# Kernel tuning notes

Measured on AMD Instinct MI355X. Metric: run time of the kernel, lower is better.

Reference implementation:

```python
import jax, jax.numpy as jnp
import numpy as np
import math

B, T, C, H = 4, 1024, 1024, 16
D = C // H
EPS = 1e-5

def layer_norm(x, gamma, beta):
    mu = jnp.mean(x, axis=-1, keepdims=True)
    var = jnp.var(x, axis=-1, keepdims=True)
    return (x - mu) * jax.lax.rsqrt(var + EPS) * gamma + beta

def setup_inputs() -> dict:
    key = jax.random.key(0)
    ks = jax.random.split(key, 12)
    s = 0.02
    return {
        "x": jax.random.normal(ks[0], (B, T, C), dtype=jnp.float32),
        "attn_mask": jax.random.randint(ks[1], (B, 1, 1, T), 0, 2, dtype=jnp.int32),
        "Wq": jax.random.normal(ks[2], (C, C), dtype=jnp.float32) * s,
        "bq": jnp.zeros((C,), dtype=jnp.float32),
        "Wk": jax.random.normal(ks[3], (C, C), dtype=jnp.float32) * s,
        "bk": jnp.zeros((C,), dtype=jnp.float32),
        "Wv": jax.random.normal(ks[4], (C, C), dtype=jnp.float32) * s,
        "bv": jnp.zeros((C,), dtype=jnp.float32),
        "Wo": jax.random.normal(ks[5], (C, C), dtype=jnp.float32) * s,
        "bo": jnp.zeros((C,), dtype=jnp.float32),
        "ln_g": jnp.ones((C,), dtype=jnp.float32),
        "ln_b": jnp.zeros((C,), dtype=jnp.float32),
    }

def reference(x, attn_mask, Wq, bq, Wk, bk, Wv, bv, Wo, bo, ln_g, ln_b):
    # projections -> [B, H, T, D]
    def split_heads(y):
        return y.reshape(B, T, H, D).transpose(0, 2, 1, 3)
    q = split_heads(x @ Wq + bq)
    k = split_heads(x @ Wk + bk)
    v = split_heads(x @ Wv + bv)
    scale = 1.0 / math.sqrt(D)
    wei = jnp.einsum('bhqd,bhkd->bhqk', q, k) * scale  # [B,H,T,T]
    wei = jnp.where(attn_mask == 0, jnp.float32(-jnp.inf), wei)
    wei = jax.nn.softmax(wei, axis=-1)
    out = jnp.einsum('bhqk,bhkd->bhqd', wei, v)
    out = out.transpose(0, 2, 1, 3).reshape(B, T, C)
    out = out @ Wo + bo
    return layer_norm(out, ln_g, ln_b)
```

## Files before the change

kernel.cpp:

```cpp
#include <hip/hip_runtime.h>
#include <stdint.h>

#define B_ 4
#define T_ 1024
#define C_ 1024
#define H_ 16
#define D_ 64
#define M_ 4096

typedef __attribute__((ext_vector_type(8))) short bf16x8;
typedef __attribute__((ext_vector_type(4))) float f32x4;
typedef __attribute__((ext_vector_type(4))) short short4v;

static __device__ __forceinline__ short f2bf(float f) {
  union { float f; unsigned u; } c; c.f = f;
  unsigned r = (c.u + 0x7fffu + ((c.u >> 16) & 1u)) >> 16;
  return (short)(unsigned short)r;
}

static __device__ __forceinline__ void gl2lds16(const void* g, void* l) {
  __builtin_amdgcn_global_load_lds(
      (const __attribute__((address_space(1))) void*)(uintptr_t)g,
      (__attribute__((address_space(3))) void*)(uint32_t)(uintptr_t)l,
      16, 0, 0);
}

__global__ __launch_bounds__(256) void k_prep(
    const float* __restrict__ x, short* __restrict__ xb,
    const float* __restrict__ Wq, const float* __restrict__ Wk,
    const float* __restrict__ Wv, const float* __restrict__ Wo,
    short* __restrict__ Wt) {
  __shared__ float t[32][33];
  const int id = blockIdx.x, tid = threadIdx.x;
  if (id < 4096) {
    int i = id * 256 + tid;
    float4 v = ((const float4*)x)[i];
    short4v o;
    o.x = f2bf(v.x); o.y = f2bf(v.y); o.z = f2bf(v.z); o.w = f2bf(v.w);
    ((short4v*)xb)[i] = o;
    return;
  }
  int j = id - 4096;
  int bz = j >> 10, r = j & 1023;
  int by = r >> 5, bx = r & 31;
  const float* W = (bz == 0) ? Wq : (bz == 1) ? Wk : (bz == 2) ? Wv : Wo;
  short* out = Wt + (size_t)bz * C_ * C_;
  int n0 = bx * 32, k0 = by * 32;
  int tx = tid & 31, ty = tid >> 5;
#pragma unroll
  for (int i = 0; i < 4; i++)
    t[ty + 8*i][tx] = W[(size_t)(k0 + ty + 8*i) * C_ + n0 + tx];
  __syncthreads();
#pragma unroll
  for (int i = 0; i < 4; i++)
    out[(size_t)(n0 + ty + 8*i) * C_ + k0 + tx] = f2bf(t[tx][ty + 8*i]);
}

static __device__ __forceinline__ void gemm_body(const short* __restrict__ A,
                                                 const short* __restrict__ Bt,
                                                 short* sA, short* sB,
                                                 f32x4 acc[4][4], int m0, int n0) {
  const int tid = threadIdx.x;
  const int w = tid >> 6, lane = tid & 63;
  const int quad = lane >> 4, l16 = lane & 15;
  const int wm = (w >> 1) * 64, wn = (w & 1) * 64;
  const int srow = lane >> 3;
  const int sch = lane & 7;

#pragma unroll
  for (int mt = 0; mt < 4; mt++)
#pragma unroll
    for (int nt = 0; nt < 4; nt++)
#pragma unroll
      for (int e = 0; e < 4; e++) acc[mt][nt][e] = 0.f;

  for (int k0 = 0; k0 < C_; k0 += 64) {
    __syncthreads();
#pragma unroll
    for (int i = 0; i < 4; i++) {
      int c = w * 4 + i;
      int row = c * 8 + srow;
      int ch = sch ^ (row & 7);
      gl2lds16(&A[(size_t)(m0 + row) * C_ + k0 + ch * 8], &sA[c * 512]);
      gl2lds16(&Bt[(size_t)(n0 + row) * C_ + k0 + ch * 8], &sB[c * 512]);
    }
    __syncthreads();
#pragma unroll
    for (int ks = 0; ks < 2; ks++) {
      bf16x8 af[4], bfv[4];
      int chq = ks * 4 + quad;
#pragma unroll
      for (int t4 = 0; t4 < 4; t4++) {
        int rowa = wm + t4 * 16 + l16;
        af[t4] = *(const bf16x8*)&sA[rowa * 64 + (chq ^ (rowa & 7)) * 8];
        int rowb = wn + t4 * 16 + l16;
        bfv[t4] = *(const bf16x8*)&sB[rowb * 64 + (chq ^ (rowb & 7)) * 8];
      }
#pragma unroll
      for (int mt = 0; mt < 4; mt++)
#pragma unroll
        for (int nt = 0; nt < 4; nt++)
          acc[mt][nt] = __builtin_amdgcn_mfma_f32_16x16x32_bf16(
              af[mt], bfv[nt], acc[mt][nt], 0, 0, 0);
    }
  }
}

__global__ __launch_bounds__(256, 3) void k_qkv(
    const short* __restrict__ A, const short* __restrict__ WtAll,
    const float* __restrict__ bq, const float* __restrict__ bk,
    const float* __restrict__ bv,
    short* __restrict__ Qb, short* __restrict__ Kb, short* __restrict__ Vtb) {
  __shared__ short sU[17408];
  const int id = blockIdx.x;
  const int mode = id % 3;
  const int j = id / 3;
  const int bx = j & 7, by = j >> 3;
  const int m0 = by * 128, n0 = bx * 128;
  const short* Bt = WtAll + (size_t)mode * C_ * C_;
  const float* bias = (mode == 0) ? bq : (mode == 1) ? bk : bv;
  f32x4 acc[4][4];
  gemm_body(A, Bt, sU, sU + 8192, acc, m0, n0);

  const int tid = threadIdx.x;
  const int w = tid >> 6, lane = tid & 63;
  const int quad = lane >> 4, l16 = lane & 15;
  const int wm = (w >> 1) * 64, wn = (w & 1) * 64;

  __syncthreads();
  if (mode < 2) {
#pragma unroll
    for (int nt = 0; nt < 4; nt++) {
      int nl = wn + nt * 16 + l16;
      float bval = bias[n0 + nl];
#pragma unroll
      for (int mt = 0; mt < 4; mt++)
#pragma unroll
        for (int r = 0; r < 4; r++)
          sU[(wm + mt * 16 + quad * 4 + r) * 136 + nl] = f2bf(acc[mt][nt][r] + bval);
    }
    __syncthreads();
    int dr = tid >> 1, hf = tid & 1;
    int mg = m0 + dr;
    int bb = mg >> 10, t = mg & 1023;
    int h = (n0 >> 6) + hf;
    short* dst = (mode == 0) ? Qb : Kb;
    size_t base = ((((size_t)(bb * H_ + h)) << 10) + t) * D_;
#pragma unroll
    for (int i = 0; i < 8; i++)
      *(int4*)&dst[base + i * 8] = *(const int4*)&sU[dr * 136 + hf * 64 + i * 8];
  } else {
#pragma unroll
    for (int nt = 0; nt < 4; nt++) {
      int nl = wn + nt * 16 + l16;
      float bval = bias[n0 + nl];
#pragma unroll
      for (int mt = 0; mt < 4; mt++)
#pragma unroll
        for (int r = 0; r < 4; r++)
          sU[nl * 136 + wm + mt * 16 + quad * 4 + r] = f2bf(acc[mt][nt][r] + bval);
    }
    __syncthreads();
    int dr = tid >> 1;
    int dg = n0 + dr, hd = dg >> 6, dl = dg & 63;
    int bb2 = m0 >> 10, t0 = m0 & 1023;
    size_t base = (((size_t)(bb2 * H_ + hd) * D_ + dl) << 10) + t0;
#pragma unroll
    for (int i = 0; i < 8; i++) {
      int jj = (tid & 1) * 8 + i;
      *(int4*)&Vtb[base + jj * 8] = *(const int4*)&sU[dr * 136 + jj * 8];
    }
  }
}

__global__ __launch_bounds__(256) void k_proj(
    const short* __restrict__ A, const short* __restrict__ Bt,
    const float* __restrict__ bias, float* __restrict__ Y) {
  __shared__ short sA[4096];
  __shared__ short sB[8192];
  const int tid = threadIdx.x;
  const int w = tid >> 6, lane = tid & 63;
  const int quad = lane >> 4, l16 = lane & 15;
  const int m0 = blockIdx.y * 64, n0 = blockIdx.x * 128;
  const int wm = (w >> 1) * 32, wn = (w & 1) * 64;
  const int srow = lane >> 3, sch = lane & 7;

  f32x4 acc[2][4];
#pragma unroll
  for (int mt = 0; mt < 2; mt++)
#pragma unroll
    for (int nt = 0; nt < 4; nt++)
#pragma unroll
      for (int e = 0; e < 4; e++) acc[mt][nt][e] = 0.f;

  for (int k0 = 0; k0 < C_; k0 += 64) {
    __syncthreads();
#pragma unroll
    for (int i = 0; i < 6; i++) {
      int c = w * 6 + i;
      if (c < 8) {
        int row = c * 8 + srow;
        int ch = sch ^ (row & 7);
        gl2lds16(&A[(size_t)(m0 + row) * C_ + k0 + ch * 8], &sA[c * 512]);
      } else {
        int c2 = c - 8;
        int row = c2 * 8 + srow;
        int ch = sch ^ (row & 7);
        gl2lds16(&Bt[(size_t)(n0 + row) * C_ + k0 + ch * 8], &sB[c2 * 512]);
      }
    }
    __syncthreads();
#pragma unroll
    for (int ks = 0; ks < 2; ks++) {
      bf16x8 af[2], bfv[4];
      int chq = ks * 4 + quad;
#pragma unroll
      for (int t2 = 0; t2 < 2; t2++) {
        int rowa = wm + t2 * 16 + l16;
        af[t2] = *(const bf16x8*)&sA[rowa * 64 + (chq ^ (rowa & 7)) * 8];
      }
#pragma unroll
      for (int t4 = 0; t4 < 4; t4++) {
        int rowb = wn + t4 * 16 + l16;
        bfv[t4] = *(const bf16x8*)&sB[rowb * 64 + (chq ^ (rowb & 7)) * 8];
      }
#pragma unroll
      for (int mt = 0; mt < 2; mt++)
#pragma unroll
        for (int nt = 0; nt < 4; nt++)
          acc[mt][nt] = __builtin_amdgcn_mfma_f32_16x16x32_bf16(
              af[mt], bfv[nt], acc[mt][nt], 0, 0, 0);
    }
  }

#pragma unroll
  for (int mt = 0; mt < 2; mt++)
#pragma unroll
    for (int nt = 0; nt < 4; nt++) {
      int ng = n0 + wn + nt * 16 + l16;
      float bval = bias[ng];
#pragma unroll
      for (int r = 0; r < 4; r++) {
        int mg = m0 + wm + mt * 16 + quad * 4 + r;
        Y[(size_t)mg * C_ + ng] = acc[mt][nt][r] + bval;
      }
    }
}

#define PSTRIDE 136
__global__ __launch_bounds__(256, 2) void k_attn(
    const short* __restrict__ Qb, const short* __restrict__ Kb,
    const short* __restrict__ Vtb, const int* __restrict__ mask,
    short* __restrict__ Ob) {
  __shared__ short sK[8192];
  __shared__ short sV[8192];
  __shared__ short sP[4 * 32 * PSTRIDE];
  __shared__ float sBias[1024];
  const int tid = threadIdx.x;
  const int w = tid >> 6, lane = tid & 63;
  const int quad = lane >> 4, l16 = lane & 15;

  const int bx = blockIdx.x;
  const int xcd = bx & 7, j = bx >> 3;
  const int qb = j & 7, u = j >> 3;
  const int h = xcd * 2 + (u & 1), bb = u >> 1;
  const int tq0 = qb * 128 + w * 32;

  const short* Qh = Qb + ((size_t)(bb * H_ + h) << 10) * D_;
  const short* Kh = Kb + ((size_t)(bb * H_ + h) << 10) * D_;
  const short* Vh = Vtb + (((size_t)(bb * H_ + h) * D_) << 10);
  const int* mrow = mask + bb * T_;
  short* Pw = &sP[w * 32 * PSTRIDE];

  const float SC = 0.125f * 1.44269504088896340736f;

  {
    int4 m4 = ((const int4*)mrow)[tid];
    float4 bv4;
    bv4.x = m4.x ? 0.f : -1e30f; bv4.y = m4.y ? 0.f : -1e30f;
    bv4.z = m4.z ? 0.f : -1e30f; bv4.w = m4.w ? 0.f : -1e30f;
    ((float4*)sBias)[tid] = bv4;
  }

  bf16x8 aq[2][2];
#pragma unroll
  for (int rt = 0; rt < 2; rt++)
#pragma unroll
    for (int ks = 0; ks < 2; ks++)
      aq[rt][ks] = *(const bf16x8*)&Qh[(size_t)(tq0 + rt * 16 + l16) * D_ +
                                       ks * 32 + quad * 8];

  f32x4 o[2][4];
  float lsum[2][4];
#pragma unroll
  for (int rt = 0; rt < 2; rt++) {
#pragma unroll
    for (int nt = 0; nt < 4; nt++)
#pragma unroll
      for (int e = 0; e < 4; e++) o[rt][nt][e] = 0.f;
#pragma unroll
    for (int r = 0; r < 4; r++) lsum[rt][r] = 0.f;
  }

  for (int kt = 0; kt < T_; kt += 128) {
    __syncthreads();
#pragma unroll
    for (int i2 = 0; i2 < 4; i2++) {
      int i = w * 4 + i2;
      int row = i * 8 + (lane >> 3);
      int g = (lane & 7) ^ (row & 7);
      gl2lds16(&Kh[(size_t)(kt + row) * D_ + g * 8], &sK[i * 512]);
    }
#pragma unroll
    for (int i2 = 0; i2 < 4; i2++) {
      int i = w * 4 + i2;
      int row = i * 4 + (lane >> 4);
      int g = (lane & 15) ^ (row & 15);
      gl2lds16(&Vh[((size_t)row << 10) + kt + g * 8], &sV[i * 512]);
    }
    __syncthreads();

    f32x4 s[2][8];
#pragma unroll
    for (int rt = 0; rt < 2; rt++)
#pragma unroll
      for (int ct = 0; ct < 8; ct++)
#pragma unroll
        for (int e = 0; e < 4; e++) s[rt][ct][e] = 0.f;

#pragma unroll
    for (int ks = 0; ks < 2; ks++)
#pragma unroll
      for (int ct = 0; ct < 8; ct++) {
        int rowb = ct * 16 + l16;
        bf16x8 bk8 = *(const bf16x8*)&sK[rowb * 64 +
                                         (((ks * 4 + quad) ^ (rowb & 7)) * 8)];
        s[0][ct] = __builtin_amdgcn_mfma_f32_16x16x32_bf16(aq[0][ks], bk8, s[0][ct], 0, 0, 0);
        s[1][ct] = __builtin_amdgcn_mfma_f32_16x16x32_bf16(aq[1][ks], bk8, s[1][ct], 0, 0, 0);
      }

    float mb[8];
#pragma unroll
    for (int ct = 0; ct < 8; ct++) mb[ct] = sBias[kt + ct * 16 + l16];

#pragma unroll
    for (int rt = 0; rt < 2; rt++)
#pragma unroll
      for (int ct = 0; ct < 8; ct++)
#pragma unroll
        for (int r = 0; r < 4; r++) {
          float p = __builtin_amdgcn_exp2f(fmaf(s[rt][ct][r], SC, mb[ct]));
          lsum[rt][r] += p;
          Pw[(rt * 16 + quad * 4 + r) * PSTRIDE + ct * 16 + l16] = f2bf(p);
        }

#pragma unroll
    for (int ks2 = 0; ks2 < 4; ks2++) {
      bf16x8 pa0 = *(const bf16x8*)&Pw[l16 * PSTRIDE + ks2 * 32 + quad * 8];
      bf16x8 pa1 = *(const bf16x8*)&Pw[(16 + l16) * PSTRIDE + ks2 * 32 + quad * 8];
#pragma unroll
      for (int nt = 0; nt < 4; nt++) {
        int rowv = nt * 16 + l16;
        bf16x8 bv8 = *(const bf16x8*)&sV[rowv * 128 +
                                         (((ks2 * 4 + quad) ^ (rowv & 15)) * 8)];
        o[0][nt] = __builtin_amdgcn_mfma_f32_16x16x32_bf16(pa0, bv8, o[0][nt], 0, 0, 0);
        o[1][nt] = __builtin_amdgcn_mfma_f32_16x16x32_bf16(pa1, bv8, o[1][nt], 0, 0, 0);
      }
    }
  }

#pragma unroll
  for (int rt = 0; rt < 2; rt++)
#pragma unroll
    for (int r = 0; r < 4; r++) {
      float rs = lsum[rt][r];
#pragma unroll
      for (int off = 1; off < 16; off <<= 1) rs += __shfl_xor(rs, off);
      float inv = 1.f / rs;
      int tg = tq0 + rt * 16 + quad * 4 + r;
#pragma unroll
      for (int nt = 0; nt < 4; nt++) {
        int col = h * D_ + nt * 16 + l16;
        Ob[(size_t)(bb * T_ + tg) * C_ + col] = f2bf(o[rt][nt][r] * inv);
      }
    }
}

__global__ __launch_bounds__(256) void k_ln(float* __restrict__ Y,
                                            const float* __restrict__ g,
                                            const float* __restrict__ b) {
  __shared__ float red[4], red2[4];
  const int row = blockIdx.x, tid = threadIdx.x;
  float4* yp = (float4*)(Y + (size_t)row * C_);
  float4 v = yp[tid];
  float sm = v.x + v.y + v.z + v.w;
#pragma unroll
  for (int off = 32; off; off >>= 1) sm += __shfl_xor(sm, off);
  if ((tid & 63) == 0) red[tid >> 6] = sm;
  __syncthreads();
  float mu = (red[0] + red[1] + red[2] + red[3]) * (1.f / C_);
  float dx = v.x - mu, dy = v.y - mu, dz = v.z - mu, dw = v.w - mu;
  float q = dx * dx + dy * dy + dz * dz + dw * dw;
#pragma unroll
  for (int off = 32; off; off >>= 1) q += __shfl_xor(q, off);
  if ((tid & 63) == 0) red2[tid >> 6] = q;
  __syncthreads();
  float var = (red2[0] + red2[1] + red2[2] + red2[3]) * (1.f / C_);
  float rsq = rsqrtf(var + 1e-5f);
  float4 gg = ((const float4*)g)[tid];
  float4 bb = ((const float4*)b)[tid];
  float4 out;
  out.x = dx * rsq * gg.x + bb.x;
  out.y = dy * rsq * gg.y + bb.y;
  out.z = dz * rsq * gg.z + bb.z;
  out.w = dw * rsq * gg.w + bb.w;
  yp[tid] = out;
}

extern "C" void kernel_launch(void* const* d_in, const int* in_sizes, int n_in,
                              void* d_out, int out_size, void* d_ws, size_t ws_size,
                              hipStream_t stream) {
  (void)in_sizes; (void)n_in; (void)out_size; (void)ws_size;
  const float* x    = (const float*)d_in[0];
  const int*   mask = (const int*)d_in[1];
  const float* Wq   = (const float*)d_in[2];
  const float* bq   = (const float*)d_in[3];
  const float* Wk   = (const float*)d_in[4];
  const float* bk   = (const float*)d_in[5];
  const float* Wv   = (const float*)d_in[6];
  const float* bv   = (const float*)d_in[7];
  const float* Wo   = (const float*)d_in[8];
  const float* bo   = (const float*)d_in[9];
  const float* lng  = (const float*)d_in[10];
  const float* lnb  = (const float*)d_in[11];

  char* ws = (char*)d_ws;
  short* xb  = (short*)(ws);
  short* Wt  = (short*)(ws + ((size_t)8  << 20));
  short* Qb  = (short*)(ws + ((size_t)16 << 20));
  short* Kb  = (short*)(ws + ((size_t)24 << 20));
  short* Vtb = (short*)(ws + ((size_t)32 << 20));
  short* Ob  = xb;
  float* Y   = (float*)d_out;

  k_prep<<<dim3(8192), dim3(256), 0, stream>>>(x, xb, Wq, Wk, Wv, Wo, Wt);
  k_qkv<<<dim3(768), dim3(256), 0, stream>>>(xb, Wt, bq, bk, bv, Qb, Kb, Vtb);
  k_attn<<<dim3(512), dim3(256), 0, stream>>>(Qb, Kb, Vtb, mask, Ob);
  k_proj<<<dim3(8, 64), dim3(256), 0, stream>>>(Ob, Wt + (size_t)3 * C_ * C_, bo, Y);
  k_ln<<<dim3(4096), dim3(256), 0, stream>>>(Y, lng, lnb);
}
```

Baseline: 186.9 us.

## Process attention row tiles sequentially to cut LDS and registers, raise occupancy

The attention kernel now handles its two 16-row query tiles one after another inside each key block, so the score accumulators and the P staging buffer cover one tile at a time. The mask bias is stored as bf16 instead of float, and the LDS P buffer is halved. Together with launch bounds raised from 2 to 3 blocks per SM, this targets lower register and LDS pressure so more waves can be resident. In exchange, each K and V fragment read from LDS now feeds one MFMA instead of two, so LDS read traffic rises. The wave also needs an in-order dependency on Pw between the two tiles, which may serialize work.

```diff
diff --git a/kernel.cpp b/kernel.cpp
--- a/kernel.cpp
+++ b/kernel.cpp
@@ -16,6 +16,10 @@
   union { float f; unsigned u; } c; c.f = f;
   unsigned r = (c.u + 0x7fffu + ((c.u >> 16) & 1u)) >> 16;
   return (short)(unsigned short)r;
+}
+static __device__ __forceinline__ float bf2f(short s) {
+  union { unsigned u; float f; } c; c.u = ((unsigned)(unsigned short)s) << 16;
+  return c.f;
 }
 
 static __device__ __forceinline__ void gl2lds16(const void* g, void* l) {
@@ -248,14 +252,14 @@
 }
 
 #define PSTRIDE 136
-__global__ __launch_bounds__(256, 2) void k_attn(
+__global__ __launch_bounds__(256, 3) void k_attn(
     const short* __restrict__ Qb, const short* __restrict__ Kb,
     const short* __restrict__ Vtb, const int* __restrict__ mask,
     short* __restrict__ Ob) {
   __shared__ short sK[8192];
   __shared__ short sV[8192];
-  __shared__ short sP[4 * 32 * PSTRIDE];
-  __shared__ float sBias[1024];
+  __shared__ short sP[4 * 16 * PSTRIDE];
+  __shared__ short sBias[1024];
   const int tid = threadIdx.x;
   const int w = tid >> 6, lane = tid & 63;
   const int quad = lane >> 4, l16 = lane & 15;
@@ -270,16 +274,18 @@
   const short* Kh = Kb + ((size_t)(bb * H_ + h) << 10) * D_;
   const short* Vh = Vtb + (((size_t)(bb * H_ + h) * D_) << 10);
   const int* mrow = mask + bb * T_;
-  short* Pw = &sP[w * 32 * PSTRIDE];
+  short* Pw = &sP[w * 16 * PSTRIDE];
 
   const float SC = 0.125f * 1.44269504088896340736f;
 
   {
     int4 m4 = ((const int4*)mrow)[tid];
-    float4 bv4;
-    bv4.x = m4.x ? 0.f : -1e30f; bv4.y = m4.y ? 0.f : -1e30f;
-    bv4.z = m4.z ? 0.f : -1e30f; bv4.w = m4.w ? 0.f : -1e30f;
-    ((float4*)sBias)[tid] = bv4;
+    short4v bv4;
+    bv4.x = m4.x ? (short)0 : f2bf(-1e30f);
+    bv4.y = m4.y ? (short)0 : f2bf(-1e30f);
+    bv4.z = m4.z ? (short)0 : f2bf(-1e30f);
+    bv4.w = m4.w ? (short)0 : f2bf(-1e30f);
+    ((short4v*)sBias)[tid] = bv4;
   }
 
   bf16x8 aq[2][2];
@@ -320,51 +326,47 @@
     }
     __syncthreads();
 
-    f32x4 s[2][8];
-#pragma unroll
-    for (int rt = 0; rt < 2; rt++)
+    float mb[8];
+#pragma unroll
+    for (int ct = 0; ct < 8; ct++) mb[ct] = bf2f(sBias[kt + ct * 16 + l16]);
+
+#pragma unroll
+    for (int rt = 0; rt < 2; rt++) {
+      f32x4 s[8];
 #pragma unroll
       for (int ct = 0; ct < 8; ct++)
 #pragma unroll
-        for (int e = 0; e < 4; e++) s[rt][ct][e] = 0.f;
-
-#pragma unroll
-    for (int ks = 0; ks < 2; ks++)
-#pragma unroll
-      for (int ct = 0; ct < 8; ct++) {
-        int rowb = ct * 16 + l16;
-        bf16x8 bk8 = *(const bf16x8*)&sK[rowb * 64 +
-                                         (((ks * 4 + quad) ^ (rowb & 7)) * 8)];
-        s[0][ct] = __builtin_amdgcn_mfma_f32_16x16x32_bf16(aq[0][ks], bk8, s[0][ct], 0, 0, 0);
-        s[1][ct] = __builtin_amdgcn_mfma_f32_16x16x32_bf16(aq[1][ks], bk8, s[1][ct], 0, 0, 0);
-      }
-
-    float mb[8];
-#pragma unroll
-    for (int ct = 0; ct < 8; ct++) mb[ct] = sBias[kt + ct * 16 + l16];
-
-#pragma unroll
-    for (int rt = 0; rt < 2; rt++)
+        for (int e = 0; e < 4; e++) s[ct][e] = 0.f;
+
+#pragma unroll
+      for (int ks = 0; ks < 2; ks++)
+#pragma unroll
+        for (int ct = 0; ct < 8; ct++) {
+          int rowb = ct * 16 + l16;
+          bf16x8 bk8 = *(const bf16x8*)&sK[rowb * 64 +
+                                           (((ks * 4 + quad) ^ (rowb & 7)) * 8)];
+          s[ct] = __builtin_amdgcn_mfma_f32_16x16x32_bf16(aq[rt][ks], bk8, s[ct], 0, 0, 0);
+        }
+
 #pragma unroll
       for (int ct = 0; ct < 8; ct++)
 #pragma unroll
         for (int r = 0; r < 4; r++) {
-          float p = __builtin_amdgcn_exp2f(fmaf(s[rt][ct][r], SC, mb[ct]));
+          float p = __builtin_amdgcn_exp2f(fmaf(s[ct][r], SC, mb[ct]));
           lsum[rt][r] += p;
-          Pw[(rt * 16 + quad * 4 + r) * PSTRIDE + ct * 16 + l16] = f2bf(p);
+          Pw[(quad * 4 + r) * PSTRIDE + ct * 16 + l16] = f2bf(p);
         }
 
 #pragma unroll
-    for (int ks2 = 0; ks2 < 4; ks2++) {
-      bf16x8 pa0 = *(const bf16x8*)&Pw[l16 * PSTRIDE + ks2 * 32 + quad * 8];
-      bf16x8 pa1 = *(const bf16x8*)&Pw[(16 + l16) * PSTRIDE + ks2 * 32 + quad * 8];
-#pragma unroll
-      for (int nt = 0; nt < 4; nt++) {
-        int rowv = nt * 16 + l16;
-        bf16x8 bv8 = *(const bf16x8*)&sV[rowv * 128 +
-                                         (((ks2 * 4 + quad) ^ (rowv & 15)) * 8)];
-        o[0][nt] = __builtin_amdgcn_mfma_f32_16x16x32_bf16(pa0, bv8, o[0][nt], 0, 0, 0);
-        o[1][nt] = __builtin_amdgcn_mfma_f32_16x16x32_bf16(pa1, bv8, o[1][nt], 0, 0, 0);
+      for (int ks2 = 0; ks2 < 4; ks2++) {
+        bf16x8 pa = *(const bf16x8*)&Pw[l16 * PSTRIDE + ks2 * 32 + quad * 8];
+#pragma unroll
+        for (int nt = 0; nt < 4; nt++) {
+          int rowv = nt * 16 + l16;
+          bf16x8 bv8 = *(const bf16x8*)&sV[rowv * 128 +
+                                           (((ks2 * 4 + quad) ^ (rowv & 15)) * 8)];
+          o[rt][nt] = __builtin_amdgcn_mfma_f32_16x16x32_bf16(pa, bv8, o[rt][nt], 0, 0, 0);
+        }
       }
     }
   }
```

Result: slower. 195.4 us (+4.6%).
